# Kernel tuning notes

Measured on AMD Instinct MI355X. Metric: run time of the kernel, lower is better.

## Reference

```python
import jax, jax.numpy as jnp
import numpy as np

THETA = 10000.0
NUM_HEADS = 16


def _rope(x, positions):
    # x: [B, H, S, Dk] (fp32), positions: [B, S] int
    d_k = x.shape[-1]
    k = jnp.arange(0, d_k, 2, dtype=jnp.float32)
    freqs = THETA ** (-k / d_k)                      # [Dk/2]
    angles = positions[..., None].astype(jnp.float32) * freqs  # [B, S, Dk/2]
    cos = jnp.cos(angles)[:, None, :, :]             # [B, 1, S, Dk/2]
    sin = jnp.sin(angles)[:, None, :, :]
    xr = x.reshape(*x.shape[:-1], d_k // 2, 2)
    x_even, x_odd = xr[..., 0], xr[..., 1]
    rot_even = x_even * cos - x_odd * sin
    rot_odd = x_even * sin + x_odd * cos
    out = jnp.stack([rot_even, rot_odd], axis=-1)
    return out.reshape(x.shape)


def setup_inputs() -> dict:
    key = jax.random.key(0)
    ks = jax.random.split(key, 6)
    B, S, D = 2, 2048, 1024
    std = (2.0 / (D + D)) ** 0.5
    x = jax.random.normal(ks[0], (B, S, D), dtype=jnp.float32)
    Wq = jax.random.normal(ks[1], (D, D), dtype=jnp.float32) * std
    Wk = jax.random.normal(ks[2], (D, D), dtype=jnp.float32) * std
    Wv = jax.random.normal(ks[3], (D, D), dtype=jnp.float32) * std
    Wo = jax.random.normal(ks[4], (D, D), dtype=jnp.float32) * std
    token_positions = jnp.broadcast_to(jnp.arange(S, dtype=jnp.int32), (B, S))
    return {"x": x, "Wq": Wq, "Wk": Wk, "Wv": Wv, "Wo": Wo,
            "token_positions": token_positions}


def reference(x, Wq, Wk, Wv, Wo, token_positions):
    B, S, D = x.shape
    H = NUM_HEADS
    Dk = D // H
    # QKV projections (no bias): y = x @ W.T
    def proj(W):
        return (x @ W.T).reshape(B, S, H, Dk).transpose(0, 2, 1, 3)  # [B,H,S,Dk]
    Q, K, V = proj(Wq), proj(Wk), proj(Wv)
    Q = _rope(Q, token_positions)
    K = _rope(K, token_positions)
    scale = 1.0 / jnp.sqrt(jnp.float32(Dk))
    scores = jnp.einsum('bhqd,bhkd->bhqk', Q, K) * scale  # [B,H,S,S]
    causal = jnp.tril(jnp.ones((S, S), dtype=bool))
    scores = jnp.where(causal, scores, -jnp.inf)
    attn = jax.nn.softmax(scores.astype(jnp.float32), axis=-1)
    out = jnp.einsum('bhqk,bhkd->bhqd', attn, V)          # [B,H,S,Dk]
    out = out.transpose(0, 2, 1, 3).reshape(B, S, D)
    return out @ Wo.T
```

## Files before the change

### kernel.cpp

```cpp
#include <hip/hip_runtime.h>
#include <math.h>

#define D_MODEL 1024
#define NHEADS 16
#define DK 64
#define SEQ 2048
#define BATCH 2
#define MROWS (BATCH * SEQ)

typedef __attribute__((ext_vector_type(8))) short bfrag8;
typedef __attribute__((ext_vector_type(4))) float f32x4;
typedef unsigned short u16;
typedef __attribute__((ext_vector_type(8))) u16 u16x8;
typedef __attribute__((ext_vector_type(4))) u16 u16x4;

#define GLOBAL_AS(p) ((const __attribute__((address_space(1))) void*)(p))
#define LDS_AS(p)    ((__attribute__((address_space(3))) void*)(p))

#define RAW_BARRIER()  __asm__ volatile("s_barrier" ::: "memory")
#define WAIT_VM8()     __asm__ volatile("s_waitcnt vmcnt(8)" ::: "memory")
#define WAIT_VM4()     __asm__ volatile("s_waitcnt vmcnt(4)" ::: "memory")
#define WAIT_VM0()     __asm__ volatile("s_waitcnt vmcnt(0)" ::: "memory")

__device__ inline u16 f2bf(float f) {
  union { float f; unsigned u; } c; c.f = f;
  unsigned r = c.u + 0x7FFF + ((c.u >> 16) & 1);
  return (u16)(r >> 16);
}

__device__ inline unsigned pack_bf2(float lo, float hi) {
  return __builtin_amdgcn_perm(__float_as_uint(hi), __float_as_uint(lo), 0x07060302);
}

struct CvtPtrs { const float* src[5]; };

__global__ __launch_bounds__(256)
void convert_and_tab(CvtPtrs p, u16* __restrict__ dst,
                     const int* __restrict__ pos, float2* __restrict__ tab) {
  const int bi = blockIdx.x;
  if (bi < 8192) {
    size_t base = ((size_t)bi * 256 + threadIdx.x) * 4;
    const size_t XSZ = (size_t)MROWS * D_MODEL;
    const float* s; size_t off;
    if (base < XSZ) { s = p.src[0]; off = base; }
    else {
      size_t j = base - XSZ;
      s = p.src[1 + (int)(j >> 20)];
      off = j & ((1u << 20) - 1);
    }
    float4 v = *(const float4*)(s + off);
    u16 o[4] = { f2bf(v.x), f2bf(v.y), f2bf(v.z), f2bf(v.w) };
    *(u16x4*)(dst + base) = *(u16x4*)o;
  } else {
    int idx = (bi - 8192) * 256 + threadIdx.x;
    int i = idx & 31, bs = idx >> 5;
    float pp = (float)pos[bs];
    float freq = expf(-(float)i * 0.2878231366242558f);
    float sn, cs;
    sincosf(pp * freq, &sn, &cs);
    tab[idx] = make_float2(cs, sn);
  }
}

__device__ inline void gemm_core(const u16* __restrict__ A, const u16* __restrict__ B,
                                 int m0, int n0, u16* As, u16* Bs,
                                 f32x4 acc[4][4]) {
  const int tid = threadIdx.x;
  const int w = tid >> 6, lane = tid & 63;
  const int l15 = lane & 15, quad = lane >> 4;
  const int wm = w >> 1, wn = w & 1;
  const int srow = tid >> 2;
  const int scol = (tid & 3) * 8;

  #pragma unroll
  for (int mi = 0; mi < 4; ++mi)
    #pragma unroll
    for (int ni = 0; ni < 4; ++ni) acc[mi][ni] = (f32x4)0.f;

  #define GSTAGE(T, BUF) do {                                                        \
    _Pragma("unroll")                                                                \
    for (int i_ = 0; i_ < 2; ++i_) {                                                 \
      const u16* ga_ = A + (size_t)((i_ * 64 + srow) + m0) * D_MODEL + (T) * 32 + scol; \
      const u16* gb_ = B + (size_t)((i_ * 64 + srow) + n0) * D_MODEL + (T) * 32 + scol; \
      __builtin_amdgcn_global_load_lds(GLOBAL_AS(ga_),                               \
          LDS_AS(&As[(BUF) * 4096 + (i_ * 64 + w * 16) * 32]), 16, 0, 0);            \
      __builtin_amdgcn_global_load_lds(GLOBAL_AS(gb_),                               \
          LDS_AS(&Bs[(BUF) * 4096 + (i_ * 64 + w * 16) * 32]), 16, 0, 0);            \
    }                                                                                \
  } while (0)

  const int NT = D_MODEL / 32;
  GSTAGE(0, 0);
  GSTAGE(1, 1);
  int sbuf = 2;
  int cbuf = 0;
  for (int t = 0; t < NT; ++t) {
    RAW_BARRIER();
    if (t + 2 < NT) {
      GSTAGE(t + 2, sbuf);
      WAIT_VM8();
    } else if (t + 1 < NT) {
      WAIT_VM4();
    } else {
      WAIT_VM0();
    }
    RAW_BARRIER();

    bfrag8 af[4], bfr[4];
    #pragma unroll
    for (int i = 0; i < 4; ++i) {
      af[i]  = *(const bfrag8*)&As[cbuf * 4096 + (wm * 64 + i * 16 + l15) * 32 + quad * 8];
      bfr[i] = *(const bfrag8*)&Bs[cbuf * 4096 + (wn * 64 + i * 16 + l15) * 32 + quad * 8];
    }
    #pragma unroll
    for (int mi = 0; mi < 4; ++mi)
      #pragma unroll
      for (int ni = 0; ni < 4; ++ni)
        acc[mi][ni] = __builtin_amdgcn_mfma_f32_16x16x32_bf16(af[mi], bfr[ni], acc[mi][ni], 0, 0, 0);

    sbuf = cbuf;
    cbuf = (cbuf == 2) ? 0 : cbuf + 1;
  }
  #undef GSTAGE
}

struct QKVArgs { const u16* A[3]; const u16* B[3]; u16* dst[3]; const float2* tab; };

__global__ __launch_bounds__(256)
void gemm_qkv_fused(QKVArgs p) {
  __shared__ u16 As[3 * 128 * 32];
  __shared__ u16 Bs[3 * 128 * 32];
  const int z = blockIdx.z;
  const int bi = blockIdx.x;
  int m0, n0;
  if (z < 2) { m0 = (bi & 7) * 128; n0 = (bi >> 3) * 128; }
  else       { m0 = (bi >> 3) * 128; n0 = (bi & 7) * 128; }
  f32x4 acc[4][4];
  gemm_core(p.A[z], p.B[z], m0, n0, As, Bs, acc);

  const int tid = threadIdx.x;
  const int w = tid >> 6, lane = tid & 63;
  const int l15 = lane & 15, quad = lane >> 4;
  const int wm = w >> 1, wn = w & 1;
  u16* dst = p.dst[z];

  if (z < 2) {
    const int head = (m0 + wm * 64) >> 6;
    const float scale = (z == 0) ? 0.125f * 1.4426950408889634f : 1.0f;
    #pragma unroll
    for (int ni = 0; ni < 4; ++ni) {
      int sg = n0 + wn * 64 + ni * 16 + l15;
      int b = sg >> 11;
      int s = sg & (SEQ - 1);
      size_t ho = ((size_t)(b * NHEADS + head)) * SEQ * DK;
      #pragma unroll
      for (int mi = 0; mi < 4; ++mi) {
        float4 t = *(const float4*)&p.tab[(size_t)sg * 32 + mi * 8 + quad * 2];
        float e0 = acc[mi][ni][0], o0 = acc[mi][ni][1];
        float e1 = acc[mi][ni][2], o1 = acc[mi][ni][3];
        u16x4 ov = { f2bf((e0 * t.x - o0 * t.y) * scale),
                     f2bf((e0 * t.y + o0 * t.x) * scale),
                     f2bf((e1 * t.z - o1 * t.w) * scale),
                     f2bf((e1 * t.w + o1 * t.z) * scale) };
        *(u16x4*)&dst[ho + (size_t)s * DK + mi * 16 + quad * 4] = ov;
      }
    }
  } else {
    const int b = m0 >> 11;
    const int head = (n0 >> 6) + wn;
    const size_t ho = ((size_t)(b * NHEADS + head)) * SEQ * DK;
    const int row_base = m0 + wm * 64;
    #pragma unroll
    for (int mi = 0; mi < 4; ++mi)
      #pragma unroll
      for (int ni = 0; ni < 4; ++ni) {
        int d = ni * 16 + l15;
        int sb = (row_base + mi * 16 + quad * 4) & (SEQ - 1);
        u16 o[4];
        #pragma unroll
        for (int r = 0; r < 4; ++r) o[r] = f2bf(acc[mi][ni][r]);
        *(u16x4*)&dst[ho + (size_t)d * SEQ + sb] = *(u16x4*)o;
      }
  }
}

__global__ __launch_bounds__(256)
void gemm_out_bf16(const u16* __restrict__ A, const u16* __restrict__ B,
                   float* __restrict__ C) {
  __shared__ u16 As[128 * 32];
  __shared__ u16 Bs[64 * 32];
  const int m0 = blockIdx.y * 128, n0 = blockIdx.x * 64;
  const int tid = threadIdx.x;
  const int w = tid >> 6, lane = tid & 63;
  const int l15 = lane & 15, quad = lane >> 4;
  const int wm = w >> 1, wn = w & 1;
  const int lrow = lane >> 2;
  const int lcol = (lane & 3) * 8;

  f32x4 acc[4][2];
  #pragma unroll
  for (int mi = 0; mi < 4; ++mi)
    #pragma unroll
    for (int ni = 0; ni < 2; ++ni) acc[mi][ni] = (f32x4)0.f;

  for (int k0 = 0; k0 < D_MODEL; k0 += 32) {
    __syncthreads();
    #pragma unroll
    for (int i = 0; i < 2; ++i) {
      int row = (i * 4 + w) * 16 + lrow;
      const u16* ga = A + (size_t)(m0 + row) * D_MODEL + k0 + lcol;
      __builtin_amdgcn_global_load_lds(GLOBAL_AS(ga), LDS_AS(&As[(i * 4 + w) * 16 * 32]), 16, 0, 0);
    }
    {
      int row = w * 16 + lrow;
      const u16* gb = B + (size_t)(n0 + row) * D_MODEL + k0 + lcol;
      __builtin_amdgcn_global_load_lds(GLOBAL_AS(gb), LDS_AS(&Bs[w * 16 * 32]), 16, 0, 0);
    }
    __syncthreads();

    bfrag8 af[4], bfr[2];
    #pragma unroll
    for (int i = 0; i < 4; ++i)
      af[i] = *(const bfrag8*)&As[(wm * 64 + i * 16 + l15) * 32 + quad * 8];
    #pragma unroll
    for (int i = 0; i < 2; ++i)
      bfr[i] = *(const bfrag8*)&Bs[(wn * 32 + i * 16 + l15) * 32 + quad * 8];
    #pragma unroll
    for (int mi = 0; mi < 4; ++mi)
      #pragma unroll
      for (int ni = 0; ni < 2; ++ni)
        acc[mi][ni] = __builtin_amdgcn_mfma_f32_16x16x32_bf16(af[mi], bfr[ni], acc[mi][ni], 0, 0, 0);
  }

  #pragma unroll
  for (int mi = 0; mi < 4; ++mi)
    #pragma unroll
    for (int ni = 0; ni < 2; ++ni)
      #pragma unroll
      for (int r = 0; r < 4; ++r) {
        int row = m0 + wm * 64 + mi * 16 + quad * 4 + r;
        int col = n0 + wn * 32 + ni * 16 + l15;
        C[(size_t)row * D_MODEL + col] = acc[mi][ni][r];
      }
}

__global__ __launch_bounds__(256, 4)
void attn_mfma(const u16* __restrict__ Qbf, const u16* __restrict__ Kbf,
               const u16* __restrict__ Vtb, u16* __restrict__ obb) {
  __shared__ u16 Ks[2][64 * 64];
  __shared__ u16 Vt[2][64 * 64];

  const int tid = threadIdx.x;
  const int w = tid >> 6, lane = tid & 63;
  const int l15 = lane & 15, quad = lane >> 4;

  const int bid = blockIdx.x;
  const int hb = bid & 31;
  const int g  = bid >> 5;
  const int tt = (g & 7) | ((g & 16) >> 1);
  const int qt = (g & 8) ? (31 - tt) : tt;
  const int b = hb >> 4, h = hb & 15;
  const size_t ho = (size_t)hb * SEQ * DK;
  const int qrow_base = qt * 64 + w * 16;

  bfrag8 qf[2];
  #pragma unroll
  for (int hh = 0; hh < 2; ++hh)
    qf[hh] = *(const bfrag8*)&Qbf[ho + (size_t)(qrow_base + l15) * DK + hh * 32 + quad * 8];

  f32x4 oacc[4];
  float l_ = 0.f;
  #pragma unroll
  for (int n0 = 0; n0 < 4; ++n0) oacc[n0] = (f32x4)0.f;

  const int srow = w * 8 + (lane >> 3);
  const int scc = ((lane & 7) ^ (srow & 7)) * 8;

  const int adr0 = (((quad & 1) << 5) + l15) << 2;
  const int adr1 = adr0 + 64;

  #define STAGE(T, BUF) do {                                                         \
    int j0_ = (T) * 64;                                                              \
    _Pragma("unroll")                                                                \
    for (int r_ = 0; r_ < 2; ++r_) {                                                 \
      int row_ = r_ * 32 + srow;                                                     \
      __builtin_amdgcn_global_load_lds(GLOBAL_AS(Kbf + ho + (size_t)(j0_ + row_) * DK + scc), \
                                       LDS_AS(&Ks[BUF][(r_ * 32 + w * 8) * 64]), 16, 0, 0);   \
      __builtin_amdgcn_global_load_lds(GLOBAL_AS(Vtb + ho + (size_t)row_ * SEQ + j0_ + scc),  \
                                       LDS_AS(&Vt[BUF][(r_ * 32 + w * 8) * 64]), 16, 0, 0);   \
    }                                                                                \
  } while (0)

  const int ntiles = qt + 1;
  STAGE(0, 0);

  for (int t = 0; t < ntiles; ++t) {
    const int j0 = t * 64;
    const int buf = t & 1;
    RAW_BARRIER();
    if (t + 1 < ntiles) {
      STAGE(t + 1, buf ^ 1);
      WAIT_VM4();
    } else {
      WAIT_VM0();
    }
    RAW_BARRIER();

    f32x4 sc[4];
    const int sw = l15 & 7;
    #pragma unroll
    for (int st = 0; st < 4; ++st) {
      int key = st * 16 + l15;
      bfrag8 kf0 = *(const bfrag8*)&Ks[buf][key * 64 + ((quad ^ sw) * 8)];
      bfrag8 kf1 = *(const bfrag8*)&Ks[buf][key * 64 + (((4 + quad) ^ sw) * 8)];
      sc[st] = __builtin_amdgcn_mfma_f32_16x16x32_bf16(kf0, qf[0], (f32x4)0.f, 0, 0, 0);
      sc[st] = __builtin_amdgcn_mfma_f32_16x16x32_bf16(kf1, qf[1], sc[st], 0, 0, 0);
    }

    if (j0 + 63 > qrow_base) {
      #pragma unroll
      for (int st = 0; st < 4; ++st)
        #pragma unroll
        for (int r = 0; r < 4; ++r) {
          int key = j0 + st * 16 + quad * 4 + r;
          if (key > qrow_base + l15) sc[st][r] = -60.f;
        }
    }

    unsigned pk[4][2];
    float rs = 0.f;
    #pragma unroll
    for (int st = 0; st < 4; ++st) {
      float p0 = __builtin_amdgcn_exp2f(fminf(sc[st][0], 60.f));
      float p1 = __builtin_amdgcn_exp2f(fminf(sc[st][1], 60.f));
      float p2 = __builtin_amdgcn_exp2f(fminf(sc[st][2], 60.f));
      float p3 = __builtin_amdgcn_exp2f(fminf(sc[st][3], 60.f));
      rs += (p0 + p1) + (p2 + p3);
      pk[st][0] = pack_bf2(p0, p1);
      pk[st][1] = pack_bf2(p2, p3);
    }
    l_ += rs;

    union PU { bfrag8 f; int i[4]; } u0, u1;
    #pragma unroll
    for (int j = 0; j < 4; ++j) {
      const int adr = (j & 2) ? adr1 : adr0;
      int lo0 = __builtin_amdgcn_ds_bpermute(adr, (int)pk[0][j & 1]);
      int hi0 = __builtin_amdgcn_ds_bpermute(adr, (int)pk[1][j & 1]);
      int lo1 = __builtin_amdgcn_ds_bpermute(adr, (int)pk[2][j & 1]);
      int hi1 = __builtin_amdgcn_ds_bpermute(adr, (int)pk[3][j & 1]);
      u0.i[j] = (quad & 2) ? hi0 : lo0;
      u1.i[j] = (quad & 2) ? hi1 : lo1;
    }
    bfrag8 pf[2] = { u0.f, u1.f };

    #pragma unroll
    for (int n0 = 0; n0 < 4; ++n0) {
      #pragma unroll
      for (int kc = 0; kc < 2; ++kc) {
        bfrag8 vf = *(const bfrag8*)&Vt[buf][(n0 * 16 + l15) * 64 + (((kc * 4 + quad) ^ sw) * 8)];
        oacc[n0] = __builtin_amdgcn_mfma_f32_16x16x32_bf16(vf, pf[kc], oacc[n0], 0, 0, 0);
      }
    }
  }
  #undef STAGE

  float l = l_;
  l += __shfl_xor(l, 16);
  l += __shfl_xor(l, 32);
  float inv = 1.f / l;
  int q = qrow_base + l15;
  #pragma unroll
  for (int n0 = 0; n0 < 4; ++n0) {
    u16x4 ov = { f2bf(oacc[n0][0] * inv), f2bf(oacc[n0][1] * inv),
                 f2bf(oacc[n0][2] * inv), f2bf(oacc[n0][3] * inv) };
    *(u16x4*)&obb[(size_t)(b * SEQ + q) * D_MODEL + h * DK + n0 * 16 + quad * 4] = ov;
  }
}

extern "C" void kernel_launch(void* const* d_in, const int* in_sizes, int n_in,
                              void* d_out, int out_size, void* d_ws, size_t ws_size,
                              hipStream_t stream) {
  const float* x  = (const float*)d_in[0];
  const float* Wq = (const float*)d_in[1];
  const float* Wk = (const float*)d_in[2];
  const float* Wv = (const float*)d_in[3];
  const float* Wo = (const float*)d_in[4];
  const int* pos  = (const int*)d_in[5];

  const size_t XSZ = (size_t)MROWS * D_MODEL;
  const size_t WSZ = (size_t)D_MODEL * D_MODEL;

  u16* bfb = (u16*)d_ws;
  u16* xb  = bfb;
  u16* wqb = xb  + XSZ;
  u16* wkb = wqb + WSZ;
  u16* wvb = wkb + WSZ;
  u16* wob = wvb + WSZ;
  u16* Qbf = wob + WSZ;
  u16* Kbf = Qbf + XSZ;
  u16* Vtb = Kbf + XSZ;
  u16* obb = Vtb + XSZ;
  float2* tab = (float2*)(obb + XSZ);

  CvtPtrs cp; cp.src[0] = x; cp.src[1] = Wq; cp.src[2] = Wk; cp.src[3] = Wv; cp.src[4] = Wo;
  convert_and_tab<<<8192 + 512, 256, 0, stream>>>(cp, xb, pos, tab);

  QKVArgs qp;
  qp.A[0] = wqb; qp.A[1] = wkb; qp.A[2] = xb;
  qp.B[0] = xb;  qp.B[1] = xb;  qp.B[2] = wvb;
  qp.dst[0] = Qbf; qp.dst[1] = Kbf; qp.dst[2] = Vtb;
  qp.tab = tab;
  gemm_qkv_fused<<<dim3(256, 1, 3), 256, 0, stream>>>(qp);

  attn_mfma<<<dim3(1024), 256, 0, stream>>>(Qbf, Kbf, Vtb, obb);

  gemm_out_bf16<<<dim3(D_MODEL / 64, MROWS / 128), 256, 0, stream>>>(obb, wob, (float*)d_out);
}
```

Baseline: 180.9 us.

## Split attention KV range across two blocks with merge; triple-buffer output GEMM

```diff
diff --git a/kernel.cpp b/kernel.cpp
--- a/kernel.cpp
+++ b/kernel.cpp
@@ -19,7 +19,9 @@
 
 #define RAW_BARRIER()  __asm__ volatile("s_barrier" ::: "memory")
 #define WAIT_VM8()     __asm__ volatile("s_waitcnt vmcnt(8)" ::: "memory")
+#define WAIT_VM6()     __asm__ volatile("s_waitcnt vmcnt(6)" ::: "memory")
 #define WAIT_VM4()     __asm__ volatile("s_waitcnt vmcnt(4)" ::: "memory")
+#define WAIT_VM3()     __asm__ volatile("s_waitcnt vmcnt(3)" ::: "memory")
 #define WAIT_VM0()     __asm__ volatile("s_waitcnt vmcnt(0)" ::: "memory")
 
 __device__ inline u16 f2bf(float f) {
@@ -187,8 +189,8 @@
 __global__ __launch_bounds__(256)
 void gemm_out_bf16(const u16* __restrict__ A, const u16* __restrict__ B,
                    float* __restrict__ C) {
-  __shared__ u16 As[128 * 32];
-  __shared__ u16 Bs[64 * 32];
+  __shared__ u16 As[3 * 128 * 32];
+  __shared__ u16 Bs[3 * 64 * 32];
   const int m0 = blockIdx.y * 128, n0 = blockIdx.x * 64;
   const int tid = threadIdx.x;
   const int w = tid >> 6, lane = tid & 63;
@@ -203,34 +205,55 @@
     #pragma unroll
     for (int ni = 0; ni < 2; ++ni) acc[mi][ni] = (f32x4)0.f;
 
-  for (int k0 = 0; k0 < D_MODEL; k0 += 32) {
-    __syncthreads();
-    #pragma unroll
-    for (int i = 0; i < 2; ++i) {
-      int row = (i * 4 + w) * 16 + lrow;
-      const u16* ga = A + (size_t)(m0 + row) * D_MODEL + k0 + lcol;
-      __builtin_amdgcn_global_load_lds(GLOBAL_AS(ga), LDS_AS(&As[(i * 4 + w) * 16 * 32]), 16, 0, 0);
-    }
-    {
-      int row = w * 16 + lrow;
-      const u16* gb = B + (size_t)(n0 + row) * D_MODEL + k0 + lcol;
-      __builtin_amdgcn_global_load_lds(GLOBAL_AS(gb), LDS_AS(&Bs[w * 16 * 32]), 16, 0, 0);
-    }
-    __syncthreads();
+  #define OSTAGE(T, BUF) do {                                                        \
+    _Pragma("unroll")                                                                \
+    for (int i_ = 0; i_ < 2; ++i_) {                                                 \
+      int row_ = (i_ * 4 + w) * 16 + lrow;                                           \
+      const u16* ga_ = A + (size_t)(m0 + row_) * D_MODEL + (T) * 32 + lcol;          \
+      __builtin_amdgcn_global_load_lds(GLOBAL_AS(ga_),                               \
+          LDS_AS(&As[(BUF) * 4096 + (i_ * 4 + w) * 16 * 32]), 16, 0, 0);             \
+    }                                                                                \
+    {                                                                                \
+      int row_ = w * 16 + lrow;                                                      \
+      const u16* gb_ = B + (size_t)(n0 + row_) * D_MODEL + (T) * 32 + lcol;          \
+      __builtin_amdgcn_global_load_lds(GLOBAL_AS(gb_),                               \
+          LDS_AS(&Bs[(BUF) * 2048 + w * 16 * 32]), 16, 0, 0);                        \
+    }                                                                                \
+  } while (0)
+
+  const int NT = D_MODEL / 32;
+  OSTAGE(0, 0);
+  OSTAGE(1, 1);
+  int sbuf = 2, cbuf = 0;
+  for (int t = 0; t < NT; ++t) {
+    RAW_BARRIER();
+    if (t + 2 < NT) {
+      OSTAGE(t + 2, sbuf);
+      WAIT_VM6();
+    } else if (t + 1 < NT) {
+      WAIT_VM3();
+    } else {
+      WAIT_VM0();
+    }
+    RAW_BARRIER();
 
     bfrag8 af[4], bfr[2];
     #pragma unroll
     for (int i = 0; i < 4; ++i)
-      af[i] = *(const bfrag8*)&As[(wm * 64 + i * 16 + l15) * 32 + quad * 8];
+      af[i] = *(const bfrag8*)&As[cbuf * 4096 + (wm * 64 + i * 16 + l15) * 32 + quad * 8];
     #pragma unroll
     for (int i = 0; i < 2; ++i)
-      bfr[i] = *(const bfrag8*)&Bs[(wn * 32 + i * 16 + l15) * 32 + quad * 8];
+      bfr[i] = *(const bfrag8*)&Bs[cbuf * 2048 + (wn * 32 + i * 16 + l15) * 32 + quad * 8];
     #pragma unroll
     for (int mi = 0; mi < 4; ++mi)
       #pragma unroll
       for (int ni = 0; ni < 2; ++ni)
         acc[mi][ni] = __builtin_amdgcn_mfma_f32_16x16x32_bf16(af[mi], bfr[ni], acc[mi][ni], 0, 0, 0);
+
+    sbuf = cbuf;
+    cbuf = (cbuf == 2) ? 0 : cbuf + 1;
   }
+  #undef OSTAGE
 
   #pragma unroll
   for (int mi = 0; mi < 4; ++mi)
@@ -246,7 +269,8 @@
 
 __global__ __launch_bounds__(256, 4)
 void attn_mfma(const u16* __restrict__ Qbf, const u16* __restrict__ Kbf,
-               const u16* __restrict__ Vtb, u16* __restrict__ obb) {
+               const u16* __restrict__ Vtb, float* __restrict__ Opart,
+               float* __restrict__ lpart) {
   __shared__ u16 Ks[2][64 * 64];
   __shared__ u16 Vt[2][64 * 64];
 
@@ -256,12 +280,17 @@
 
   const int bid = blockIdx.x;
   const int hb = bid & 31;
-  const int g  = bid >> 5;
+  const int half = (bid >> 5) & 1;
+  const int g = bid >> 6;
   const int tt = (g & 7) | ((g & 16) >> 1);
   const int qt = (g & 8) ? (31 - tt) : tt;
-  const int b = hb >> 4, h = hb & 15;
   const size_t ho = (size_t)hb * SEQ * DK;
   const int qrow_base = qt * 64 + w * 16;
+
+  const int n = qt + 1;
+  const int mid = (n + 1) >> 1;
+  const int lo = half ? mid : 0;
+  const int hi = half ? n : mid;
 
   bfrag8 qf[2];
   #pragma unroll
@@ -291,75 +320,75 @@
     }                                                                                \
   } while (0)
 
-  const int ntiles = qt + 1;
-  STAGE(0, 0);
-
-  for (int t = 0; t < ntiles; ++t) {
-    const int j0 = t * 64;
-    const int buf = t & 1;
-    RAW_BARRIER();
-    if (t + 1 < ntiles) {
-      STAGE(t + 1, buf ^ 1);
-      WAIT_VM4();
-    } else {
-      WAIT_VM0();
-    }
-    RAW_BARRIER();
-
-    f32x4 sc[4];
-    const int sw = l15 & 7;
-    #pragma unroll
-    for (int st = 0; st < 4; ++st) {
-      int key = st * 16 + l15;
-      bfrag8 kf0 = *(const bfrag8*)&Ks[buf][key * 64 + ((quad ^ sw) * 8)];
-      bfrag8 kf1 = *(const bfrag8*)&Ks[buf][key * 64 + (((4 + quad) ^ sw) * 8)];
-      sc[st] = __builtin_amdgcn_mfma_f32_16x16x32_bf16(kf0, qf[0], (f32x4)0.f, 0, 0, 0);
-      sc[st] = __builtin_amdgcn_mfma_f32_16x16x32_bf16(kf1, qf[1], sc[st], 0, 0, 0);
-    }
-
-    if (j0 + 63 > qrow_base) {
-      #pragma unroll
-      for (int st = 0; st < 4; ++st)
+  if (hi > lo) {
+    STAGE(lo, 0);
+    for (int t = lo; t < hi; ++t) {
+      const int j0 = t * 64;
+      const int buf = (t - lo) & 1;
+      RAW_BARRIER();
+      if (t + 1 < hi) {
+        STAGE(t + 1, buf ^ 1);
+        WAIT_VM4();
+      } else {
+        WAIT_VM0();
+      }
+      RAW_BARRIER();
+
+      f32x4 sc[4];
+      const int sw = l15 & 7;
+      #pragma unroll
+      for (int st = 0; st < 4; ++st) {
+        int key = st * 16 + l15;
+        bfrag8 kf0 = *(const bfrag8*)&Ks[buf][key * 64 + ((quad ^ sw) * 8)];
+        bfrag8 kf1 = *(const bfrag8*)&Ks[buf][key * 64 + (((4 + quad) ^ sw) * 8)];
+        sc[st] = __builtin_amdgcn_mfma_f32_16x16x32_bf16(kf0, qf[0], (f32x4)0.f, 0, 0, 0);
+        sc[st] = __builtin_amdgcn_mfma_f32_16x16x32_bf16(kf1, qf[1], sc[st], 0, 0, 0);
+      }
+
+      if (j0 + 63 > qrow_base) {
         #pragma unroll
-        for (int r = 0; r < 4; ++r) {
-          int key = j0 + st * 16 + quad * 4 + r;
-          if (key > qrow_base + l15) sc[st][r] = -60.f;
+        for (int st = 0; st < 4; ++st)
+          #pragma unroll
+          for (int r = 0; r < 4; ++r) {
+            int key = j0 + st * 16 + quad * 4 + r;
+            if (key > qrow_base + l15) sc[st][r] = -60.f;
+          }
+      }
+
+      unsigned pk[4][2];
+      float rs = 0.f;
+      #pragma unroll
+      for (int st = 0; st < 4; ++st) {
+        float p0 = __builtin_amdgcn_exp2f(fminf(sc[st][0], 60.f));
+        float p1 = __builtin_amdgcn_exp2f(fminf(sc[st][1], 60.f));
+        float p2 = __builtin_amdgcn_exp2f(fminf(sc[st][2], 60.f));
+        float p3 = __builtin_amdgcn_exp2f(fminf(sc[st][3], 60.f));
+        rs += (p0 + p1) + (p2 + p3);
+        pk[st][0] = pack_bf2(p0, p1);
+        pk[st][1] = pack_bf2(p2, p3);
+      }
+      l_ += rs;
+
+      union PU { bfrag8 f; int i[4]; } u0, u1;
+      #pragma unroll
+      for (int j = 0; j < 4; ++j) {
+        const int adr = (j & 2) ? adr1 : adr0;
+        int lo0 = __builtin_amdgcn_ds_bpermute(adr, (int)pk[0][j & 1]);
+        int hi0 = __builtin_amdgcn_ds_bpermute(adr, (int)pk[1][j & 1]);
+        int lo1 = __builtin_amdgcn_ds_bpermute(adr, (int)pk[2][j & 1]);
+        int hi1 = __builtin_amdgcn_ds_bpermute(adr, (int)pk[3][j & 1]);
+        u0.i[j] = (quad & 2) ? hi0 : lo0;
+        u1.i[j] = (quad & 2) ? hi1 : lo1;
+      }
+      bfrag8 pf[2] = { u0.f, u1.f };
+
+      #pragma unroll
+      for (int n0 = 0; n0 < 4; ++n0) {
+        #pragma unroll
+        for (int kc = 0; kc < 2; ++kc) {
+          bfrag8 vf = *(const bfrag8*)&Vt[buf][(n0 * 16 + l15) * 64 + (((kc * 4 + quad) ^ sw) * 8)];
+          oacc[n0] = __builtin_amdgcn_mfma_f32_16x16x32_bf16(vf, pf[kc], oacc[n0], 0, 0, 0);
         }
-    }
-
-    unsigned pk[4][2];
-    float rs = 0.f;
-    #pragma unroll
-    for (int st = 0; st < 4; ++st) {
-      float p0 = __builtin_amdgcn_exp2f(fminf(sc[st][0], 60.f));
-      float p1 = __builtin_amdgcn_exp2f(fminf(sc[st][1], 60.f));
-      float p2 = __builtin_amdgcn_exp2f(fminf(sc[st][2], 60.f));
-      float p3 = __builtin_amdgcn_exp2f(fminf(sc[st][3], 60.f));
-      rs += (p0 + p1) + (p2 + p3);
-      pk[st][0] = pack_bf2(p0, p1);
-      pk[st][1] = pack_bf2(p2, p3);
-    }
-    l_ += rs;
-
-    union PU { bfrag8 f; int i[4]; } u0, u1;
-    #pragma unroll
-    for (int j = 0; j < 4; ++j) {
-      const int adr = (j & 2) ? adr1 : adr0;
-      int lo0 = __builtin_amdgcn_ds_bpermute(adr, (int)pk[0][j & 1]);
-      int hi0 = __builtin_amdgcn_ds_bpermute(adr, (int)pk[1][j & 1]);
-      int lo1 = __builtin_amdgcn_ds_bpermute(adr, (int)pk[2][j & 1]);
-      int hi1 = __builtin_amdgcn_ds_bpermute(adr, (int)pk[3][j & 1]);
-      u0.i[j] = (quad & 2) ? hi0 : lo0;
-      u1.i[j] = (quad & 2) ? hi1 : lo1;
-    }
-    bfrag8 pf[2] = { u0.f, u1.f };
-
-    #pragma unroll
-    for (int n0 = 0; n0 < 4; ++n0) {
-      #pragma unroll
-      for (int kc = 0; kc < 2; ++kc) {
-        bfrag8 vf = *(const bfrag8*)&Vt[buf][(n0 * 16 + l15) * 64 + (((kc * 4 + quad) ^ sw) * 8)];
-        oacc[n0] = __builtin_amdgcn_mfma_f32_16x16x32_bf16(vf, pf[kc], oacc[n0], 0, 0, 0);
       }
     }
   }
@@ -368,14 +397,30 @@
   float l = l_;
   l += __shfl_xor(l, 16);
   l += __shfl_xor(l, 32);
+  int q = qrow_base + l15;
+  float* Op = Opart + ((size_t)(half * 32 + hb) * SEQ + q) * DK;
+  #pragma unroll
+  for (int n0 = 0; n0 < 4; ++n0)
+    *(f32x4*)&Op[n0 * 16 + quad * 4] = oacc[n0];
+  if (quad == 0)
+    lpart[(size_t)(half * 32 + hb) * SEQ + q] = l;
+}
+
+__global__ __launch_bounds__(256)
+void attn_merge(const float* __restrict__ Opart, const float* __restrict__ lpart,
+                u16* __restrict__ obb) {
+  int idx = blockIdx.x * 256 + threadIdx.x;
+  int t = idx & 15;
+  int q = (idx >> 4) & (SEQ - 1);
+  int hb = idx >> 15;
+  int b = hb >> 4, h = hb & 15;
+  float l = lpart[(size_t)hb * SEQ + q] + lpart[(size_t)(32 + hb) * SEQ + q];
   float inv = 1.f / l;
-  int q = qrow_base + l15;
-  #pragma unroll
-  for (int n0 = 0; n0 < 4; ++n0) {
-    u16x4 ov = { f2bf(oacc[n0][0] * inv), f2bf(oacc[n0][1] * inv),
-                 f2bf(oacc[n0][2] * inv), f2bf(oacc[n0][3] * inv) };
-    *(u16x4*)&obb[(size_t)(b * SEQ + q) * D_MODEL + h * DK + n0 * 16 + quad * 4] = ov;
-  }
+  f32x4 a = *(const f32x4*)(Opart + ((size_t)hb * SEQ + q) * DK + t * 4);
+  f32x4 c = *(const f32x4*)(Opart + ((size_t)(32 + hb) * SEQ + q) * DK + t * 4);
+  u16x4 ov = { f2bf((a[0] + c[0]) * inv), f2bf((a[1] + c[1]) * inv),
+               f2bf((a[2] + c[2]) * inv), f2bf((a[3] + c[3]) * inv) };
+  *(u16x4*)&obb[((size_t)(b * SEQ + q)) * D_MODEL + h * DK + t * 4] = ov;
 }
 
 extern "C" void kernel_launch(void* const* d_in, const int* in_sizes, int n_in,
@@ -402,6 +447,8 @@
   u16* Vtb = Kbf + XSZ;
   u16* obb = Vtb + XSZ;
   float2* tab = (float2*)(obb + XSZ);
+  float* Opart = (float*)(tab + 131072);
+  float* lpart = Opart + (size_t)2 * 32 * SEQ * DK;
 
   CvtPtrs cp; cp.src[0] = x; cp.src[1] = Wq; cp.src[2] = Wk; cp.src[3] = Wv; cp.src[4] = Wo;
   convert_and_tab<<<8192 + 512, 256, 0, stream>>>(cp, xb, pos, tab);
@@ -413,7 +460,9 @@
   qp.tab = tab;
   gemm_qkv_fused<<<dim3(256, 1, 3), 256, 0, stream>>>(qp);
 
-  attn_mfma<<<dim3(1024), 256, 0, stream>>>(Qbf, Kbf, Vtb, obb);
+  attn_mfma<<<dim3(2048), 256, 0, stream>>>(Qbf, Kbf, Vtb, Opart, lpart);
+
+  attn_merge<<<dim3(4096), 256, 0, stream>>>(Opart, lpart, obb);
 
   gemm_out_bf16<<<dim3(D_MODEL / 64, MROWS / 128), 256, 0, stream>>>(obb, wob, (float*)d_out);
 }
```

Result: slower. 188.6 us (+4.3%).

## Split attention key tiles across two wave groups with LDS reduction

Applied to the files above, without the earlier changes.

```diff
diff --git a/kernel.cpp b/kernel.cpp
--- a/kernel.cpp
+++ b/kernel.cpp
@@ -20,6 +20,7 @@
 #define RAW_BARRIER()  __asm__ volatile("s_barrier" ::: "memory")
 #define WAIT_VM8()     __asm__ volatile("s_waitcnt vmcnt(8)" ::: "memory")
 #define WAIT_VM4()     __asm__ volatile("s_waitcnt vmcnt(4)" ::: "memory")
+#define WAIT_VM2()     __asm__ volatile("s_waitcnt vmcnt(2)" ::: "memory")
 #define WAIT_VM0()     __asm__ volatile("s_waitcnt vmcnt(0)" ::: "memory")
 
 __device__ inline u16 f2bf(float f) {
@@ -244,7 +245,7 @@
       }
 }
 
-__global__ __launch_bounds__(256, 4)
+__global__ __launch_bounds__(512, 8)
 void attn_mfma(const u16* __restrict__ Qbf, const u16* __restrict__ Kbf,
                const u16* __restrict__ Vtb, u16* __restrict__ obb) {
   __shared__ u16 Ks[2][64 * 64];
@@ -253,6 +254,7 @@
   const int tid = threadIdx.x;
   const int w = tid >> 6, lane = tid & 63;
   const int l15 = lane & 15, quad = lane >> 4;
+  const int wq = w & 3, kh = w >> 2;
 
   const int bid = blockIdx.x;
   const int hb = bid & 31;
@@ -261,7 +263,7 @@
   const int qt = (g & 8) ? (31 - tt) : tt;
   const int b = hb >> 4, h = hb & 15;
   const size_t ho = (size_t)hb * SEQ * DK;
-  const int qrow_base = qt * 64 + w * 16;
+  const int qrow_base = qt * 64 + wq * 16;
 
   bfrag8 qf[2];
   #pragma unroll
@@ -274,21 +276,17 @@
   for (int n0 = 0; n0 < 4; ++n0) oacc[n0] = (f32x4)0.f;
 
   const int srow = w * 8 + (lane >> 3);
-  const int scc = ((lane & 7) ^ (srow & 7)) * 8;
+  const int scc = ((lane & 7) ^ ((lane >> 3) & 7)) * 8;
 
   const int adr0 = (((quad & 1) << 5) + l15) << 2;
   const int adr1 = adr0 + 64;
 
   #define STAGE(T, BUF) do {                                                         \
     int j0_ = (T) * 64;                                                              \
-    _Pragma("unroll")                                                                \
-    for (int r_ = 0; r_ < 2; ++r_) {                                                 \
-      int row_ = r_ * 32 + srow;                                                     \
-      __builtin_amdgcn_global_load_lds(GLOBAL_AS(Kbf + ho + (size_t)(j0_ + row_) * DK + scc), \
-                                       LDS_AS(&Ks[BUF][(r_ * 32 + w * 8) * 64]), 16, 0, 0);   \
-      __builtin_amdgcn_global_load_lds(GLOBAL_AS(Vtb + ho + (size_t)row_ * SEQ + j0_ + scc),  \
-                                       LDS_AS(&Vt[BUF][(r_ * 32 + w * 8) * 64]), 16, 0, 0);   \
-    }                                                                                \
+    __builtin_amdgcn_global_load_lds(GLOBAL_AS(Kbf + ho + (size_t)(j0_ + srow) * DK + scc), \
+                                     LDS_AS(&Ks[BUF][w * 512]), 16, 0, 0);           \
+    __builtin_amdgcn_global_load_lds(GLOBAL_AS(Vtb + ho + (size_t)srow * SEQ + j0_ + scc),  \
+                                     LDS_AS(&Vt[BUF][w * 512]), 16, 0, 0);           \
   } while (0)
 
   const int ntiles = qt + 1;
@@ -300,17 +298,17 @@
     RAW_BARRIER();
     if (t + 1 < ntiles) {
       STAGE(t + 1, buf ^ 1);
-      WAIT_VM4();
+      WAIT_VM2();
     } else {
       WAIT_VM0();
     }
     RAW_BARRIER();
 
-    f32x4 sc[4];
+    f32x4 sc[2];
     const int sw = l15 & 7;
     #pragma unroll
-    for (int st = 0; st < 4; ++st) {
-      int key = st * 16 + l15;
+    for (int st = 0; st < 2; ++st) {
+      int key = kh * 32 + st * 16 + l15;
       bfrag8 kf0 = *(const bfrag8*)&Ks[buf][key * 64 + ((quad ^ sw) * 8)];
       bfrag8 kf1 = *(const bfrag8*)&Ks[buf][key * 64 + (((4 + quad) ^ sw) * 8)];
       sc[st] = __builtin_amdgcn_mfma_f32_16x16x32_bf16(kf0, qf[0], (f32x4)0.f, 0, 0, 0);
@@ -319,18 +317,18 @@
 
     if (j0 + 63 > qrow_base) {
       #pragma unroll
-      for (int st = 0; st < 4; ++st)
+      for (int st = 0; st < 2; ++st)
         #pragma unroll
         for (int r = 0; r < 4; ++r) {
-          int key = j0 + st * 16 + quad * 4 + r;
+          int key = j0 + kh * 32 + st * 16 + quad * 4 + r;
           if (key > qrow_base + l15) sc[st][r] = -60.f;
         }
     }
 
-    unsigned pk[4][2];
+    unsigned pk[2][2];
     float rs = 0.f;
     #pragma unroll
-    for (int st = 0; st < 4; ++st) {
+    for (int st = 0; st < 2; ++st) {
       float p0 = __builtin_amdgcn_exp2f(fminf(sc[st][0], 60.f));
       float p1 = __builtin_amdgcn_exp2f(fminf(sc[st][1], 60.f));
       float p2 = __builtin_amdgcn_exp2f(fminf(sc[st][2], 60.f));
@@ -341,26 +339,20 @@
     }
     l_ += rs;
 
-    union PU { bfrag8 f; int i[4]; } u0, u1;
+    union PU { bfrag8 f; int i[4]; } u0;
     #pragma unroll
     for (int j = 0; j < 4; ++j) {
       const int adr = (j & 2) ? adr1 : adr0;
       int lo0 = __builtin_amdgcn_ds_bpermute(adr, (int)pk[0][j & 1]);
       int hi0 = __builtin_amdgcn_ds_bpermute(adr, (int)pk[1][j & 1]);
-      int lo1 = __builtin_amdgcn_ds_bpermute(adr, (int)pk[2][j & 1]);
-      int hi1 = __builtin_amdgcn_ds_bpermute(adr, (int)pk[3][j & 1]);
       u0.i[j] = (quad & 2) ? hi0 : lo0;
-      u1.i[j] = (quad & 2) ? hi1 : lo1;
-    }
-    bfrag8 pf[2] = { u0.f, u1.f };
+    }
+    bfrag8 pf = u0.f;
 
     #pragma unroll
     for (int n0 = 0; n0 < 4; ++n0) {
-      #pragma unroll
-      for (int kc = 0; kc < 2; ++kc) {
-        bfrag8 vf = *(const bfrag8*)&Vt[buf][(n0 * 16 + l15) * 64 + (((kc * 4 + quad) ^ sw) * 8)];
-        oacc[n0] = __builtin_amdgcn_mfma_f32_16x16x32_bf16(vf, pf[kc], oacc[n0], 0, 0, 0);
-      }
+      bfrag8 vf = *(const bfrag8*)&Vt[buf][(n0 * 16 + l15) * 64 + (((kh * 4 + quad) ^ sw) * 8)];
+      oacc[n0] = __builtin_amdgcn_mfma_f32_16x16x32_bf16(vf, pf, oacc[n0], 0, 0, 0);
     }
   }
   #undef STAGE
@@ -368,13 +360,28 @@
   float l = l_;
   l += __shfl_xor(l, 16);
   l += __shfl_xor(l, 32);
-  float inv = 1.f / l;
-  int q = qrow_base + l15;
-  #pragma unroll
-  for (int n0 = 0; n0 < 4; ++n0) {
-    u16x4 ov = { f2bf(oacc[n0][0] * inv), f2bf(oacc[n0][1] * inv),
-                 f2bf(oacc[n0][2] * inv), f2bf(oacc[n0][3] * inv) };
-    *(u16x4*)&obb[(size_t)(b * SEQ + q) * D_MODEL + h * DK + n0 * 16 + quad * 4] = ov;
+
+  RAW_BARRIER();
+  float* osc = (float*)Ks;
+  float* lsc = (float*)Vt;
+  if (kh == 1) {
+    #pragma unroll
+    for (int n0 = 0; n0 < 4; ++n0)
+      *(f32x4*)&osc[(wq * 64 + lane) * 16 + n0 * 4] = oacc[n0];
+    if (quad == 0) lsc[wq * 16 + l15] = l;
+  }
+  RAW_BARRIER();
+  if (kh == 0) {
+    float lt = l + lsc[wq * 16 + l15];
+    float inv = 1.f / lt;
+    int q = qrow_base + l15;
+    #pragma unroll
+    for (int n0 = 0; n0 < 4; ++n0) {
+      f32x4 o2 = *(const f32x4*)&osc[(wq * 64 + lane) * 16 + n0 * 4];
+      u16x4 ov = { f2bf((oacc[n0][0] + o2[0]) * inv), f2bf((oacc[n0][1] + o2[1]) * inv),
+                   f2bf((oacc[n0][2] + o2[2]) * inv), f2bf((oacc[n0][3] + o2[3]) * inv) };
+      *(u16x4*)&obb[(size_t)(b * SEQ + q) * D_MODEL + h * DK + n0 * 16 + quad * 4] = ov;
+    }
   }
 }
 
@@ -413,7 +420,7 @@
   qp.tab = tab;
   gemm_qkv_fused<<<dim3(256, 1, 3), 256, 0, stream>>>(qp);
 
-  attn_mfma<<<dim3(1024), 256, 0, stream>>>(Qbf, Kbf, Vtb, obb);
+  attn_mfma<<<dim3(1024), 512, 0, stream>>>(Qbf, Kbf, Vtb, obb);
 
   gemm_out_bf16<<<dim3(D_MODEL / 64, MROWS / 128), 256, 0, stream>>>(obb, wob, (float*)d_out);
 }
```

New measurement: 179.8 us. No clear change (-0.6%).
